# Performance work log

Measured on AMD Instinct MI355X. Metric: run time of the kernel, lower is better.

Reference implementation:

```python
import jax, jax.numpy as jnp
import numpy as np

N, H, B, SS = 8192, 128, 64, 20


def _rate(z_a, z_b, k_idx, psi, W_om, b_om):
    # z_a, z_b: [..., H]; k_idx: int [...] event-type selector
    Wsel = W_om[k_idx]                    # [..., 2H]
    bsel = b_om[k_idx]
    psel = psi[k_idx]
    zab = jnp.concatenate([z_a, z_b], -1)
    zba = jnp.concatenate([z_b, z_a], -1)
    g = 0.5 * ((zab * Wsel).sum(-1) + bsel + (zba * Wsel).sum(-1) + bsel)
    x = jnp.clip(g / psel, -75.0, 75.0)
    return psel * jnp.log1p(jnp.exp(x))  # psi * log(1 + exp(g/psi))


def _forward(u, v, t, k, u_others, v_others, A, S, embeddings, last_event_time,
             W_S, W_R, W_t, W_h, b_h, psi, W_om, b_om):
    # 1) event intensities lambda_uvk  [B]
    lam = _rate(embeddings[u], embeddings[v], k, psi, W_om, b_om)
    # 2) survival loss. Replicates the original accumulation (incl. the
    #    v_surv = u_surv + rate_v overwrite bug): L_surv = sum_ev (2*(ru0+ru1)+rv1)/SS, shape [SS]
    z_u = embeddings[u][:, None, :]       # [B,1,H]
    z_v = embeddings[v][:, None, :]
    z_vo = embeddings[v_others]           # [B,SS,H]
    z_uo = embeddings[u_others]
    zub = jnp.broadcast_to(z_u, z_vo.shape)
    zvb = jnp.broadcast_to(z_v, z_uo.shape)
    k0 = jnp.zeros((B, SS), jnp.int32)
    k1 = jnp.ones((B, SS), jnp.int32)
    ru0 = _rate(zub, z_vo, k0, psi, W_om, b_om)
    ru1 = _rate(zub, z_vo, k1, psi, W_om, b_om)
    rv1 = _rate(zvb, z_uo, k1, psi, W_om, b_om)
    L_surv = (2.0 * (ru0 + ru1) + rv1).sum(0) / SS
    # 3) sequential per-event embedding update (the kernel-headroom part)
    def step(carry, ev):
        z, let = carry
        ui, vi, ti = ev
        h = z @ W_h.T + b_h               # [N,H] W_h applied to z_previous
        def side(n1, n2):
            dt = ti - let[n1]
            mask = A[n2] > 0              # neighbors of n2
            q = jnp.exp(S[n2]) * mask
            q = q / (q.sum() + 1e-7)
            vals = jnp.where(mask[:, None], jax.nn.sigmoid(q[:, None] * h), -jnp.inf)
            hs = jnp.where(mask.any(), vals.max(0), 0.0)   # max over neighbors
            return dt, hs
        dt0, hs0 = side(ui, vi)
        dt1, hs1 = side(vi, ui)
        dts = jnp.stack([dt0, dt1])       # [2]
        hstruct = jnp.stack([hs0, hs1])   # [2,H]
        L = hstruct @ W_S.T
        # original indexes z_prev[[n1,n2]] AFTER the inner loop, i.e. [v,u]
        rows = jnp.stack([vi, ui])
        Sterm = z[rows] @ W_R.T
        E = dts[:, None] * W_t[:, 0][None, :]   # Linear(1,H) on time deltas
        z = z.at[rows].set(jax.nn.sigmoid(L + Sterm + E))
        let = let.at[ui].set(ti).at[vi].set(ti)
        return (z, let), None
    (z_final, _), _ = jax.lax.scan(step, (embeddings, last_event_time), (u, v, t))
    return lam, L_surv, z_final


def setup_inputs():
    ks = jax.random.split(jax.random.key(0), 16)
    u = jax.random.randint(ks[0], (B,), 0, N)
    v = jax.random.randint(ks[1], (B,), 0, N)
    t = jnp.sort(jax.random.uniform(ks[2], (B,), jnp.float32) * 100.0)
    k = jax.random.randint(ks[3], (B,), 0, 2)
    u_others = jax.random.randint(ks[4], (B, SS), 0, N)
    v_others = jax.random.randint(ks[5], (B, SS), 0, N)
    Au = jax.random.uniform(ks[6], (N, N)) < (16.0 / N)   # avg degree ~16
    A = jnp.maximum(Au, Au.T).astype(jnp.float32)
    S = A / jnp.clip(A.sum(1, keepdims=True), 1.0)        # degree-normalized init
    embeddings = jax.random.uniform(ks[7], (N, H), jnp.float32)
    last_event_time = jnp.zeros((N,), jnp.float32)
    sc = 1.0 / np.sqrt(H)
    def lin(key, shape, s=sc):
        return jax.random.uniform(key, shape, jnp.float32, -s, s)
    W_S = lin(ks[8], (H, H)); W_R = lin(ks[9], (H, H))
    W_t = lin(ks[10], (H, 1)); W_h = lin(ks[11], (H, H)); b_h = lin(ks[12], (H,))
    psi = 0.5 * jnp.ones((2,), jnp.float32)
    sc2 = 1.0 / np.sqrt(2 * H)
    W_om = jax.random.uniform(ks[13], (2, 2 * H), jnp.float32, -sc2, sc2)
    b_om = jax.random.uniform(ks[14], (2,), jnp.float32, -sc2, sc2)
    return dict(u=u, v=v, t=t, k=k, u_others=u_others, v_others=v_others,
                A=A, S=S, embeddings=embeddings, last_event_time=last_event_time,
                W_S=W_S, W_R=W_R, W_t=W_t, W_h=W_h, b_h=b_h,
                psi=psi, W_om=W_om, b_om=b_om)


def reference(u, v, t, k, u_others, v_others, A, S, embeddings, last_event_time,
              W_S, W_R, W_t, W_h, b_h, psi, W_om, b_om):
    return _forward(u, v, t, k, u_others, v_others, A, S, embeddings, last_event_time,
                    W_S, W_R, W_t, W_h, b_h, psi, W_om, b_om)
```

## Files before the change

kernel.cpp:

```cpp
#include <hip/hip_runtime.h>
#include <math.h>

#define N 8192
#define H 128
#define NEV 64
#define SS 20
#define MAXD 512
#define MAXDIRTY 128
#define RPB 32
#define SPIN_GUARD (1 << 18)

__global__ __launch_bounds__(512) void k_emb(
    const float* __restrict__ emb, const float* __restrict__ W_h,
    const float* __restrict__ b_h, const float* __restrict__ W_om,
    float* __restrict__ h_tab, float* __restrict__ z_out,
    float* __restrict__ d0, float* __restrict__ d1,
    unsigned long long* __restrict__ donebits)
{
    const int tid = threadIdx.x;
    const int c = tid & 127;
    const int s = tid >> 7;
    const int r0 = blockIdx.x * RPB;

    if (blockIdx.x == 0 && tid == 0) donebits[0] = 0ull;

    __shared__ __align__(16) float z4[4 * 128];
    __shared__ float pr[8 * 128];

    float whr[32];
#pragma unroll
    for (int i = 0; i < 32; ++i) whr[i] = W_h[c * H + s * 32 + i];
    const float bh_c = b_h[c];

    const int lane = tid & 63;
    const int wid = tid >> 6;
    const int kof = (wid >= 4) ? 256 : 0;
    const float wk_l = W_om[kof + lane]      + W_om[kof + 128 + lane];
    const float wk_h = W_om[kof + 64 + lane] + W_om[kof + 192 + lane];

    for (int b = 0; b < RPB / 4; ++b) {
        const int rbase = r0 + b * 4;
        __syncthreads();
        const float zv = emb[(size_t)rbase * H + tid];
        z4[tid] = zv;
        z_out[(size_t)rbase * H + tid] = zv;
        __syncthreads();

#pragma unroll
        for (int rr = 0; rr < 4; ++rr) {
            float a = 0.f;
#pragma unroll
            for (int i4 = 0; i4 < 8; ++i4) {
                const float4 zz = *(const float4*)&z4[rr * 128 + s * 32 + i4 * 4];
                a += zz.x * whr[i4 * 4] + zz.y * whr[i4 * 4 + 1] +
                     zz.z * whr[i4 * 4 + 2] + zz.w * whr[i4 * 4 + 3];
            }
            pr[(s * 4 + rr) * 128 + c] = a;
        }
        {
            const int rr = wid & 3;
            float val = z4[rr * 128 + lane] * wk_l + z4[rr * 128 + 64 + lane] * wk_h;
#pragma unroll
            for (int off = 32; off > 0; off >>= 1) val += __shfl_xor(val, off);
            if (lane == 0) {
                if (wid < 4) d0[rbase + rr] = val;
                else         d1[rbase + rr] = val;
            }
        }
        __syncthreads();
        {
            const int rr = s;
            const float h = pr[(0 * 4 + rr) * 128 + c] + pr[(1 * 4 + rr) * 128 + c] +
                            pr[(2 * 4 + rr) * 128 + c] + pr[(3 * 4 + rr) * 128 + c] + bh_c;
            h_tab[(size_t)(rbase + rr) * H + c] = h;
        }
    }
}

__global__ __launch_bounds__(512) void k_parls(
    const int* __restrict__ u, const int* __restrict__ v,
    const float* __restrict__ t, const int* __restrict__ kk,
    const int* __restrict__ u_o, const int* __restrict__ v_o,
    const float* __restrict__ lastt, const float* __restrict__ emb,
    const float* __restrict__ A, const float* __restrict__ S,
    const float* __restrict__ h_tab,
    const float* __restrict__ W_S, const float* __restrict__ W_R,
    const float* __restrict__ W_t, const float* __restrict__ W_h,
    const float* __restrict__ b_h,
    const float* __restrict__ psi, const float* __restrict__ b_om,
    const float* __restrict__ d0, const float* __restrict__ d1,
    float* __restrict__ z_slot, float* __restrict__ h_slot,
    unsigned long long* __restrict__ donebits,
    float* __restrict__ lamout, float* __restrict__ svout,
    float* __restrict__ z_out)
{
    const int bid = blockIdx.x;
    const int tid = threadIdx.x;

    if (bid >= NEV) {
        if (bid == NEV) {
            if (tid < NEV) {
                const int b = tid;
                const int kv = kk[b];
                const float* dk = kv ? d1 : d0;
                const float g = 0.5f * (dk[u[b]] + dk[v[b]]) + b_om[kv];
                const float ps = psi[kv];
                const float x = fminf(75.f, fmaxf(-75.f, g / ps));
                lamout[b] = ps * log1pf(expf(x));
            }
        } else {
            const int s = bid - NEV - 1;
            if (tid < 64) {
                const int b = tid;
                const float p0 = psi[0], p1 = psi[1], bo0 = b_om[0], bo1 = b_om[1];
                const int vo = v_o[b * SS + s], uo = u_o[b * SS + s];
                float g, x;
                g = 0.5f * (d0[u[b]] + d0[vo]) + bo0; x = fminf(75.f, fmaxf(-75.f, g / p0));
                const float ru0 = p0 * log1pf(expf(x));
                g = 0.5f * (d1[u[b]] + d1[vo]) + bo1; x = fminf(75.f, fmaxf(-75.f, g / p1));
                const float ru1 = p1 * log1pf(expf(x));
                g = 0.5f * (d1[v[b]] + d1[uo]) + bo1; x = fminf(75.f, fmaxf(-75.f, g / p1));
                const float rv1 = p1 * log1pf(expf(x));
                float val = 2.f * (ru0 + ru1) + rv1;
#pragma unroll
                for (int off = 32; off > 0; off >>= 1) val += __shfl_xor(val, off);
                if (b == 0) svout[s] = val / (float)SS;
            }
        }
        return;
    }

    const int e = bid;
    const int r = (tid >> 7) & 1;
    const int c = tid & 127;
    const int slot = 2 * e + r;

    __shared__ int   uL[NEV], vL[NEV];
    __shared__ int   nbr_i[MAXD];
    __shared__ float nbr_e[MAXD];
    __shared__ int   flagL[MAXD];
    __shared__ float rs[512];
    __shared__ float redm[512];
    __shared__ float msA[2][128];
    __shared__ int   dlsA[2][MAXDIRTY];
    __shared__ float dlqA[2][MAXDIRTY];
    __shared__ int   dcA[2], degA[2];
    __shared__ int   cntL, dcL;
    __shared__ float sumL;
    __shared__ __align__(16) float hs_s[2][128];
    __shared__ __align__(16) float zz_s[2][128];
    __shared__ __align__(16) float zn_s[2][128];
    __shared__ int   zdepL[2], lastupL[2], nodeL[2];
    __shared__ float dtvL[2];
    __shared__ unsigned long long need_s;

    if (tid < NEV)          uL[tid] = u[tid];
    else if (tid < 2 * NEV) vL[tid - NEV] = v[tid - NEV];
    __syncthreads();

    if (tid < 2) {
        const int sl = 2 * e + tid;
        const int node = tid ? uL[e] : vL[e];
        nodeL[tid] = node;
        int zd = -1;
        for (int j = 2 * e - 1; j >= 0; --j) {
            const int nj = (j & 1) ? uL[j >> 1] : vL[j >> 1];
            if (nj == node) { zd = j; break; }
        }
        zdepL[tid] = zd;
        int lu = 1;
        for (int j = sl + 1; j < 2 * NEV; ++j) {
            const int nj = (j & 1) ? uL[j >> 1] : vL[j >> 1];
            if (nj == node) { lu = 0; break; }
        }
        lastupL[tid] = lu;
        const int dtn = tid ? vL[e] : uL[e];
        int pt = -1;
        for (int e2 = e - 1; e2 >= 0; --e2)
            if (uL[e2] == dtn || vL[e2] == dtn) { pt = e2; break; }
        const float lv = (pt >= 0) ? t[pt] : lastt[dtn];
        dtvL[tid] = t[e] - lv;
    }
    __syncthreads();

    for (int sl = 0; sl < 2; ++sl) {
        const int row = sl ? uL[e] : vL[e];
        const size_t base = (size_t)row * N;
        if (tid == 0) { cntL = 0; dcL = 0; }
        __syncthreads();

        float lsum = 0.f;
        {
            const float4* A4 = (const float4*)(A + base);
            for (int j4 = tid; j4 < N / 4; j4 += 512) {
                const float4 a4 = A4[j4];
#pragma unroll
                for (int q = 0; q < 4; ++q) {
                    const float av = (q == 0) ? a4.x : (q == 1) ? a4.y
                                   : (q == 2) ? a4.z : a4.w;
                    if (av > 0.f) {
                        const int j = 4 * j4 + q;
                        const float ev = expf(S[base + j]);
                        lsum += ev;
                        const int p = atomicAdd(&cntL, 1);
                        if (p < MAXD) { nbr_i[p] = j; nbr_e[p] = ev; }
                    }
                }
            }
        }
        rs[tid] = lsum;
        __syncthreads();
        for (int off = 256; off > 0; off >>= 1) {
            if (tid < off) rs[tid] += rs[tid + off];
            __syncthreads();
        }
        if (tid == 0) { sumL = rs[0]; degA[sl] = cntL; }
        __syncthreads();

        const int d = min(cntL, MAXD);
        const float rinv = 1.f / (sumL + 1e-7f);

        for (int j0 = tid; j0 < d; j0 += 512) {
            const int j = nbr_i[j0];
            int dep = -1;
            for (int s2 = 2 * e - 1; s2 >= 0; --s2) {
                const int nj = (s2 & 1) ? uL[s2 >> 1] : vL[s2 >> 1];
                if (nj == j) { dep = s2; break; }
            }
            flagL[j0] = dep;
        }
        __syncthreads();

        {
            const int cc = tid & 127, quarter = tid >> 7;
            float m = -INFINITY;
            for (int j0 = quarter; j0 < d; j0 += 4) {
                if (flagL[j0] < 0)
                    m = fmaxf(m, nbr_e[j0] * rinv * h_tab[(size_t)nbr_i[j0] * H + cc]);
            }
            redm[tid] = m;
            __syncthreads();
            if (tid < 128)
                msA[sl][cc] = fmaxf(fmaxf(redm[cc], redm[128 + cc]),
                                    fmaxf(redm[256 + cc], redm[384 + cc]));
        }

        for (int j0 = tid; j0 < d; j0 += 512) {
            const int dep = flagL[j0];
            if (dep >= 0) {
                const int p = atomicAdd(&dcL, 1);
                if (p < MAXDIRTY) { dlsA[sl][p] = dep; dlqA[sl][p] = nbr_e[j0] * rinv; }
            }
        }
        __syncthreads();
        if (tid == 0) dcA[sl] = dcL;
        __syncthreads();
    }

    if (tid == 0) {
        unsigned long long need = 0ull;
        for (int rr = 0; rr < 2; ++rr) {
            const int zd = zdepL[rr];
            if (zd >= 0) need |= 1ull << (zd >> 1);
            const int dn = min(dcA[rr], MAXDIRTY);
            for (int p = 0; p < dn; ++p)
                need |= 1ull << (dlsA[rr][p] >> 1);
        }
        need_s = need;
        if (need) {
            int guard = 0;
            while ((__hip_atomic_load(donebits, __ATOMIC_ACQUIRE,
                                      __HIP_MEMORY_SCOPE_AGENT) & need) != need) {
                __builtin_amdgcn_s_sleep(2);
                if (++guard > SPIN_GUARD) break;
            }
        }
    }
    __syncthreads();
    if (need_s) {
        unsigned long long db = __hip_atomic_load(donebits, __ATOMIC_ACQUIRE,
                                                  __HIP_MEMORY_SCOPE_AGENT);
        (void)db;
    }

    if (tid < 256) {
        float m = msA[r][c];
        const int dn = min(dcA[r], MAXDIRTY);
        for (int p = 0; p < dn; ++p) {
            const int ds = dlsA[r][p];
            const float q = dlqA[r][p];
            m = fmaxf(m, q * h_slot[ds * H + c]);
        }
        hs_s[r][c] = (degA[r] > 0) ? 1.f / (1.f + __expf(-m)) : 0.f;
        const int zd = zdepL[r];
        zz_s[r][c] = (zd >= 0) ? z_slot[zd * H + c]
                               : emb[(size_t)nodeL[r] * H + c];
    }
    __syncthreads();

    if (tid < 256) {
        float g = 0.f;
        const float4* ws4 = (const float4*)(W_S + (size_t)c * H);
        const float4* wr4 = (const float4*)(W_R + (size_t)c * H);
#pragma unroll
        for (int i = 0; i < 32; ++i) {
            const float4 a = ws4[i];
            const float4 b = wr4[i];
            const float4 hh = *(const float4*)&hs_s[r][4 * i];
            const float4 zz = *(const float4*)&zz_s[r][4 * i];
            g += hh.x * a.x + hh.y * a.y + hh.z * a.z + hh.w * a.w +
                 zz.x * b.x + zz.y * b.y + zz.z * b.z + zz.w * b.w;
        }
        g += dtvL[r] * W_t[c];
        const float zv = 1.f / (1.f + __expf(-g));
        zn_s[r][c] = zv;
        z_slot[slot * H + c] = zv;
        if (lastupL[r])
            z_out[(size_t)nodeL[r] * H + c] = zv;
    }
    __syncthreads();

    if (tid < 256) {
        float h = 0.f;
        const float4* wh4 = (const float4*)(W_h + (size_t)c * H);
#pragma unroll
        for (int i = 0; i < 32; ++i) {
            const float4 a = wh4[i];
            const float4 zz = *(const float4*)&zn_s[r][4 * i];
            h += zz.x * a.x + zz.y * a.y + zz.z * a.z + zz.w * a.w;
        }
        h_slot[slot * H + c] = h + b_h[c];
    }

    __syncthreads();
    if (tid == 0) {
        __threadfence();
        __hip_atomic_fetch_or(donebits, 1ull << e, __ATOMIC_RELEASE,
                              __HIP_MEMORY_SCOPE_AGENT);
    }
}

extern "C" void kernel_launch(void* const* d_in, const int* in_sizes, int n_in,
                              void* d_out, int out_size, void* d_ws, size_t ws_size,
                              hipStream_t stream)
{
    const int*   u        = (const int*)d_in[0];
    const int*   v        = (const int*)d_in[1];
    const float* t        = (const float*)d_in[2];
    const int*   k        = (const int*)d_in[3];
    const int*   u_others = (const int*)d_in[4];
    const int*   v_others = (const int*)d_in[5];
    const float* A        = (const float*)d_in[6];
    const float* S        = (const float*)d_in[7];
    const float* emb      = (const float*)d_in[8];
    const float* lastt    = (const float*)d_in[9];
    const float* W_S      = (const float*)d_in[10];
    const float* W_R      = (const float*)d_in[11];
    const float* W_t      = (const float*)d_in[12];
    const float* W_h      = (const float*)d_in[13];
    const float* b_h      = (const float*)d_in[14];
    const float* psi      = (const float*)d_in[15];
    const float* W_om     = (const float*)d_in[16];
    const float* b_om     = (const float*)d_in[17];
    (void)in_sizes; (void)n_in; (void)out_size; (void)ws_size;

    float* wsf    = (float*)d_ws;
    float* h_tab  = wsf;
    float* d0     = h_tab + (size_t)N * H;
    float* d1     = d0 + N;
    float* Mstat  = d1 + N;
    float* dl_q   = Mstat + 128 * H;
    float* z_slot = dl_q + 128 * MAXDIRTY;
    float* h_slot = z_slot + 128 * H;
    int*   deg    = (int*)(h_slot + 128 * H);
    int*   dcnt   = deg + 128;
    int*   dl_s   = dcnt + 128;
    unsigned long long* donebits = (unsigned long long*)(dl_s + 128 * MAXDIRTY);

    float* out    = (float*)d_out;
    float* lamout = out;
    float* svout  = out + NEV;
    float* z_out  = out + NEV + SS;

    k_emb<<<N / RPB, 512, 0, stream>>>(emb, W_h, b_h, W_om, h_tab, z_out,
                                       d0, d1, donebits);
    k_parls<<<NEV + 1 + SS, 512, 0, stream>>>(u, v, t, k, u_others, v_others,
                                              lastt, emb, A, S, h_tab,
                                              W_S, W_R, W_t, W_h, b_h,
                                              psi, b_om, d0, d1,
                                              z_slot, h_slot, donebits,
                                              lamout, svout, z_out);
}
```

Before: 99.91 us.

## Process both neighbor rows concurrently with half-blocks and halve rows per embedding block

Result: faster. 94.32 us (-5.6%).

```diff
diff --git a/kernel.cpp b/kernel.cpp
--- a/kernel.cpp
+++ b/kernel.cpp
@@ -7,7 +7,7 @@
 #define SS 20
 #define MAXD 512
 #define MAXDIRTY 128
-#define RPB 32
+#define RPB 16
 #define SPIN_GUARD (1 << 18)
 
 __global__ __launch_bounds__(512) void k_emb(
@@ -134,19 +134,20 @@
     const int r = (tid >> 7) & 1;
     const int c = tid & 127;
     const int slot = 2 * e + r;
+    const int half = tid >> 8;
+    const int ht = tid & 255;
 
     __shared__ int   uL[NEV], vL[NEV];
-    __shared__ int   nbr_i[MAXD];
-    __shared__ float nbr_e[MAXD];
-    __shared__ int   flagL[MAXD];
+    __shared__ int   nbr2[2][MAXD];
+    __shared__ float nbe2[2][MAXD];
+    __shared__ int   flag2[2][MAXD];
     __shared__ float rs[512];
     __shared__ float redm[512];
     __shared__ float msA[2][128];
     __shared__ int   dlsA[2][MAXDIRTY];
     __shared__ float dlqA[2][MAXDIRTY];
-    __shared__ int   dcA[2], degA[2];
-    __shared__ int   cntL, dcL;
-    __shared__ float sumL;
+    __shared__ int   dcA[2], degA[2], cntA[2];
+    __shared__ float sumA[2];
     __shared__ __align__(16) float hs_s[2][128];
     __shared__ __align__(16) float zz_s[2][128];
     __shared__ __align__(16) float zn_s[2][128];
@@ -156,6 +157,7 @@
 
     if (tid < NEV)          uL[tid] = u[tid];
     else if (tid < 2 * NEV) vL[tid - NEV] = v[tid - NEV];
+    if (tid < 2) { cntA[tid] = 0; dcA[tid] = 0; }
     __syncthreads();
 
     if (tid < 2) {
@@ -183,16 +185,14 @@
     }
     __syncthreads();
 
-    for (int sl = 0; sl < 2; ++sl) {
-        const int row = sl ? uL[e] : vL[e];
-        const size_t base = (size_t)row * N;
-        if (tid == 0) { cntL = 0; dcL = 0; }
-        __syncthreads();
+    {
+        const int rowN = half ? uL[e] : vL[e];
+        const size_t baseN = (size_t)rowN * N;
 
         float lsum = 0.f;
         {
-            const float4* A4 = (const float4*)(A + base);
-            for (int j4 = tid; j4 < N / 4; j4 += 512) {
+            const float4* A4 = (const float4*)(A + baseN);
+            for (int j4 = ht; j4 < N / 4; j4 += 256) {
                 const float4 a4 = A4[j4];
 #pragma unroll
                 for (int q = 0; q < 4; ++q) {
@@ -200,60 +200,59 @@
                                    : (q == 2) ? a4.z : a4.w;
                     if (av > 0.f) {
                         const int j = 4 * j4 + q;
-                        const float ev = expf(S[base + j]);
+                        const float ev = expf(S[baseN + j]);
                         lsum += ev;
-                        const int p = atomicAdd(&cntL, 1);
-                        if (p < MAXD) { nbr_i[p] = j; nbr_e[p] = ev; }
+                        const int p = atomicAdd(&cntA[half], 1);
+                        if (p < MAXD) { nbr2[half][p] = j; nbe2[half][p] = ev; }
                     }
                 }
             }
         }
         rs[tid] = lsum;
         __syncthreads();
-        for (int off = 256; off > 0; off >>= 1) {
-            if (tid < off) rs[tid] += rs[tid + off];
+        for (int off = 128; off > 0; off >>= 1) {
+            if (ht < off) rs[tid] += rs[tid + off];
             __syncthreads();
         }
-        if (tid == 0) { sumL = rs[0]; degA[sl] = cntL; }
-        __syncthreads();
-
-        const int d = min(cntL, MAXD);
-        const float rinv = 1.f / (sumL + 1e-7f);
-
-        for (int j0 = tid; j0 < d; j0 += 512) {
-            const int j = nbr_i[j0];
+        if (ht == 0) { sumA[half] = rs[tid]; degA[half] = cntA[half]; }
+        __syncthreads();
+
+        const int dH = min(cntA[half], MAXD);
+        const float rinvH = 1.f / (sumA[half] + 1e-7f);
+
+        for (int j0 = ht; j0 < dH; j0 += 256) {
+            const int j = nbr2[half][j0];
             int dep = -1;
             for (int s2 = 2 * e - 1; s2 >= 0; --s2) {
                 const int nj = (s2 & 1) ? uL[s2 >> 1] : vL[s2 >> 1];
                 if (nj == j) { dep = s2; break; }
             }
-            flagL[j0] = dep;
+            flag2[half][j0] = dep;
         }
         __syncthreads();
 
         {
-            const int cc = tid & 127, quarter = tid >> 7;
+            const int cc = ht & 127, pr2 = ht >> 7;
             float m = -INFINITY;
-            for (int j0 = quarter; j0 < d; j0 += 4) {
-                if (flagL[j0] < 0)
-                    m = fmaxf(m, nbr_e[j0] * rinv * h_tab[(size_t)nbr_i[j0] * H + cc]);
+            for (int j0 = pr2; j0 < dH; j0 += 2) {
+                if (flag2[half][j0] < 0)
+                    m = fmaxf(m, nbe2[half][j0] * rinvH *
+                              h_tab[(size_t)nbr2[half][j0] * H + cc]);
             }
             redm[tid] = m;
             __syncthreads();
-            if (tid < 128)
-                msA[sl][cc] = fmaxf(fmaxf(redm[cc], redm[128 + cc]),
-                                    fmaxf(redm[256 + cc], redm[384 + cc]));
-        }
-
-        for (int j0 = tid; j0 < d; j0 += 512) {
-            const int dep = flagL[j0];
+            if (ht < 128)
+                msA[half][cc] = fmaxf(redm[half * 256 + cc],
+                                      redm[half * 256 + 128 + cc]);
+        }
+
+        for (int j0 = ht; j0 < dH; j0 += 256) {
+            const int dep = flag2[half][j0];
             if (dep >= 0) {
-                const int p = atomicAdd(&dcL, 1);
-                if (p < MAXDIRTY) { dlsA[sl][p] = dep; dlqA[sl][p] = nbr_e[j0] * rinv; }
-            }
-        }
-        __syncthreads();
-        if (tid == 0) dcA[sl] = dcL;
+                const int p = atomicAdd(&dcA[half], 1);
+                if (p < MAXDIRTY) { dlsA[half][p] = dep; dlqA[half][p] = nbe2[half][j0] * rinvH; }
+            }
+        }
         __syncthreads();
     }
 
```
